# Performance work log

Hardware: AMD Instinct MI355X
Metric: run time of the kernel (lower is better)

Reference implementation:

```python
import jax, jax.numpy as jnp
import numpy as np


def setup_inputs() -> dict:
    key = jax.random.key(0)
    ks = jax.random.split(key, 6)
    B, U, E, D, P = 8, 1024, 1024, 256, 256
    return {
        "u_enc": jax.random.normal(ks[0], (B, U, D), dtype=jnp.float32),
        "e_enc": jax.random.normal(ks[1], (B, E, D), dtype=jnp.float32),
        "pair_enc": jax.random.normal(ks[2], (B, U, E), dtype=jnp.float32),
        "ue_mask": jax.random.uniform(ks[3], (B, U, E), dtype=jnp.float32),
        "w_kernel": jax.random.normal(ks[4], (D, P), dtype=jnp.float32) / np.sqrt(D).astype(np.float32),
        "w_bias": jnp.zeros((P,), dtype=jnp.float32),
        "bpp_w": jnp.ones((), dtype=jnp.float32),
        "bpp_b": jnp.zeros((), dtype=jnp.float32),
    }


def reference(u_enc, e_enc, pair_enc, ue_mask, w_kernel, w_bias, bpp_w, bpp_b):
    # OuterProductUpdate: shared Dense projection of u and e, then outer product.
    u_p = u_enc @ w_kernel + w_bias            # [B,U,P]
    e_p = e_enc @ w_kernel + w_bias            # [B,E,P]
    op = ue_mask * jnp.einsum('bup,bep->bue', u_p, e_p)  # [B,U,E]
    # Sigmoid gate over pair features.
    mask = ue_mask * jax.nn.sigmoid(bpp_w * pair_enc + bpp_b + op)  # [B,U,E]
    # Original: (mask[...,None] * concat(u_rep, e_rep)).sum(axis=(-2,-3)).
    # Algebraically identical without the UxEx2D intermediate:
    #   concat( sum_{u,e} mask * u_enc[u],  sum_{u,e} mask * e_enc[e] )
    u_part = jnp.einsum('bue,bud->bd', mask, u_enc)  # [B,D]
    e_part = jnp.einsum('bue,bed->bd', mask, e_enc)  # [B,D]
    return jnp.concatenate([u_part, e_part], axis=-1)  # [B,2D]
```

## Files before the change

### kernel.cpp

```cpp
#include <hip/hip_runtime.h>

#define BDIM 8
#define UDIM 1024
#define EDIM 1024
#define DDIM 256
#define PDIM 256

typedef __attribute__((ext_vector_type(8))) short bf16x8;
typedef __attribute__((ext_vector_type(4))) float f32x4;

__device__ __forceinline__ short f2bf(float x) {
    unsigned u = __float_as_uint(x);
    unsigned r = (u + 0x7FFFu + ((u >> 16) & 1u)) >> 16;
    return (short)r;
}

__global__ __launch_bounds__(256) void prep_kernel(
    const float* __restrict__ w, ushort* __restrict__ wT,
    float* __restrict__ sums ,
    float* __restrict__ out, int out_size)
{
    int n = blockIdx.x, k = threadIdx.x;
    wT[(size_t)n * PDIM + k] = (ushort)f2bf(w[(size_t)k * PDIM + n]);
    int g = n * 256 + k;
    if (g < BDIM * UDIM + BDIM * EDIM) sums[g] = 0.f;
    if (g < out_size) out[g] = 0.f;
}

__global__ __launch_bounds__(256) void proj_kernel(
    const float* __restrict__ u_enc, const float* __restrict__ e_enc,
    const ushort* __restrict__ wT, const float* __restrict__ bias,
    ushort* __restrict__ u_p, ushort* __restrict__ e_p)
{
    int row0 = blockIdx.x * 64;
    int col0 = blockIdx.y * 64;
    const float* A; ushort* C;
    if (row0 < BDIM * UDIM) { A = u_enc; C = u_p; }
    else                    { A = e_enc; C = e_p; row0 -= BDIM * UDIM; }

    int tid  = threadIdx.x;
    int wave = tid >> 6, lane = tid & 63;
    int m = lane & 15, quad = lane >> 4;

    const float* aptr = A + (size_t)(row0 + wave * 16 + m) * DDIM + quad * 8;

    f32x4 acc[4] = {};

    #pragma unroll
    for (int k0 = 0; k0 < DDIM; k0 += 32) {
        float4 a0 = *(const float4*)(aptr + k0);
        float4 a1 = *(const float4*)(aptr + k0 + 4);
        bf16x8 af;
        af[0] = f2bf(a0.x); af[1] = f2bf(a0.y); af[2] = f2bf(a0.z); af[3] = f2bf(a0.w);
        af[4] = f2bf(a1.x); af[5] = f2bf(a1.y); af[6] = f2bf(a1.z); af[7] = f2bf(a1.w);
        #pragma unroll
        for (int nt = 0; nt < 4; ++nt) {
            bf16x8 bfr = *(const bf16x8*)(wT + (size_t)(col0 + nt * 16 + m) * DDIM + k0 + quad * 8);
            acc[nt] = __builtin_amdgcn_mfma_f32_16x16x32_bf16(af, bfr, acc[nt], 0, 0, 0);
        }
    }

    #pragma unroll
    for (int nt = 0; nt < 4; ++nt) {
        int col = col0 + nt * 16 + m;
        float bv = bias[col];
        #pragma unroll
        for (int r = 0; r < 4; ++r) {
            int row = row0 + wave * 16 + quad * 4 + r;
            C[(size_t)row * PDIM + col] = (ushort)f2bf(acc[nt][r] + bv);
        }
    }
}

__global__ __launch_bounds__(256) void fused_kernel(
    const ushort* __restrict__ u_p, const ushort* __restrict__ e_p,
    const float* __restrict__ pair_enc, const float* __restrict__ ue_mask,
    const float* __restrict__ bpp_w_p, const float* __restrict__ bpp_b_p,
    float* __restrict__ row_sums, float* __restrict__ col_sums)
{
    __shared__ float colred[4][64];

    int b  = blockIdx.y;
    int iu = blockIdx.x >> 4, ie = blockIdx.x & 15;
    int u0 = iu * 64, e0 = ie * 64;

    int tid  = threadIdx.x;
    int wave = tid >> 6, lane = tid & 63;
    int m = lane & 15, quad = lane >> 4;

    const ushort* Au = u_p + (size_t)b * UDIM * PDIM + (size_t)(u0 + wave * 16 + m) * PDIM + quad * 8;
    const ushort* Be = e_p + (size_t)b * EDIM * PDIM + (size_t)(e0 + m) * PDIM + quad * 8;

    f32x4 acc[4] = {};

    #pragma unroll
    for (int k0 = 0; k0 < PDIM; k0 += 32) {
        bf16x8 af = *(const bf16x8*)(Au + k0);
        #pragma unroll
        for (int nt = 0; nt < 4; ++nt) {
            bf16x8 bfr = *(const bf16x8*)(Be + (size_t)nt * 16 * PDIM + k0);
            acc[nt] = __builtin_amdgcn_mfma_f32_16x16x32_bf16(af, bfr, acc[nt], 0, 0, 0);
        }
    }

    float bw = bpp_w_p[0], bb = bpp_b_p[0];
    const float* pm = pair_enc + (size_t)b * UDIM * EDIM;
    const float* mm = ue_mask  + (size_t)b * UDIM * EDIM;

    float rsum[4] = {0.f, 0.f, 0.f, 0.f};
    float csum[4] = {0.f, 0.f, 0.f, 0.f};
    #pragma unroll
    for (int r = 0; r < 4; ++r) {
        int row = u0 + wave * 16 + quad * 4 + r;
        #pragma unroll
        for (int nt = 0; nt < 4; ++nt) {
            int col = e0 + nt * 16 + m;
            size_t idx = (size_t)row * EDIM + col;
            float mv = mm[idx], pv = pm[idx];
            float arg = bw * pv + bb + mv * acc[nt][r];
            float s = mv / (1.f + __expf(-arg));
            rsum[r]  += s;
            csum[nt] += s;
        }
    }

    #pragma unroll
    for (int r = 0; r < 4; ++r) {
        float v = rsum[r];
        v += __shfl_xor(v, 1); v += __shfl_xor(v, 2);
        v += __shfl_xor(v, 4); v += __shfl_xor(v, 8);
        if (m == 0)
            atomicAdd(&row_sums[(size_t)b * UDIM + u0 + wave * 16 + quad * 4 + r], v);
    }

    #pragma unroll
    for (int nt = 0; nt < 4; ++nt) {
        float v = csum[nt];
        v += __shfl_xor(v, 16); v += __shfl_xor(v, 32);
        if (quad == 0) colred[wave][nt * 16 + m] = v;
    }
    __syncthreads();

    if (tid < 64) {
        float v = colred[0][tid] + colred[1][tid] + colred[2][tid] + colred[3][tid];
        atomicAdd(&col_sums[(size_t)b * EDIM + e0 + tid], v);
    }
}

__global__ __launch_bounds__(256) void finish_kernel(
    const float* __restrict__ u_enc, const float* __restrict__ e_enc,
    const float* __restrict__ row_sums, const float* __restrict__ col_sums,
    float* __restrict__ out)
{
    int b = blockIdx.x;
    int half = blockIdx.y;
    int chunk = blockIdx.z;
    int d = threadIdx.x;

    const float* enc = half ? e_enc : u_enc;
    const float* s   = half ? col_sums : row_sums;

    int base = chunk * 64;
    float acc = 0.f;
    #pragma unroll 4
    for (int u = 0; u < 64; ++u) {
        float sv = s[(size_t)b * UDIM + base + u];
        acc += sv * enc[(size_t)(b * UDIM + base + u) * DDIM + d];
    }
    atomicAdd(&out[(size_t)b * 2 * DDIM + half * DDIM + d], acc);
}

extern "C" void kernel_launch(void* const* d_in, const int* in_sizes, int n_in,
                              void* d_out, int out_size, void* d_ws, size_t ws_size,
                              hipStream_t stream)
{
    const float* u_enc    = (const float*)d_in[0];
    const float* e_enc    = (const float*)d_in[1];
    const float* pair_enc = (const float*)d_in[2];
    const float* ue_mask  = (const float*)d_in[3];
    const float* w_kernel = (const float*)d_in[4];
    const float* w_bias   = (const float*)d_in[5];
    const float* bpp_w    = (const float*)d_in[6];
    const float* bpp_b    = (const float*)d_in[7];
    float* out = (float*)d_out;

    ushort* u_p = (ushort*)d_ws;
    ushort* e_p = u_p + (size_t)BDIM * UDIM * PDIM;
    ushort* wT  = e_p + (size_t)BDIM * EDIM * PDIM;
    float* row_sums = (float*)(wT + (size_t)DDIM * PDIM);
    float* col_sums = row_sums + BDIM * UDIM;

    prep_kernel<<<dim3(256), 256, 0, stream>>>(w_kernel, wT, row_sums, out, out_size);

    proj_kernel<<<dim3(256, 4), 256, 0, stream>>>(u_enc, e_enc, wT, w_bias, u_p, e_p);

    fused_kernel<<<dim3(256, BDIM), 256, 0, stream>>>(u_p, e_p, pair_enc, ue_mask,
                                                      bpp_w, bpp_b, row_sums, col_sums);

    finish_kernel<<<dim3(BDIM, 2, 16), 256, 0, stream>>>(u_enc, e_enc, row_sums, col_sums, out);
}
```

Baseline: 180.0 us.

## Prefetch operands into registers and remap block order across all kernels

Every kernel now issues its global loads up front into register arrays. That covers the A rows in proj, the u_p fragments and the pair/mask tiles in fused, and the encoder rows in finish, so memory latency overlaps instead of serializing with the MFMA and sigmoid work. proj and fused use a 1D grid with swizzled block indices so the 8 XCDs each get a batch-local slice, which should improve L2 locality. prep transposes four columns per thread with float4 loads, and finish splits into more chunks for parallelism. The cost is higher register pressure and more atomics in finish.

```diff
diff --git a/kernel.cpp b/kernel.cpp
--- a/kernel.cpp
+++ b/kernel.cpp
@@ -20,10 +20,15 @@
     float* __restrict__ sums ,
     float* __restrict__ out, int out_size)
 {
-    int n = blockIdx.x, k = threadIdx.x;
-    wT[(size_t)n * PDIM + k] = (ushort)f2bf(w[(size_t)k * PDIM + n]);
-    int g = n * 256 + k;
-    if (g < BDIM * UDIM + BDIM * EDIM) sums[g] = 0.f;
+    int k  = threadIdx.x;
+    int n0 = blockIdx.x * 4;
+    float4 wv = *(const float4*)(w + (size_t)k * PDIM + n0);
+    wT[(size_t)(n0 + 0) * DDIM + k] = (ushort)f2bf(wv.x);
+    wT[(size_t)(n0 + 1) * DDIM + k] = (ushort)f2bf(wv.y);
+    wT[(size_t)(n0 + 2) * DDIM + k] = (ushort)f2bf(wv.z);
+    wT[(size_t)(n0 + 3) * DDIM + k] = (ushort)f2bf(wv.w);
+    int g = blockIdx.x * 256 + k;
+    sums[g] = 0.f;
     if (g < out_size) out[g] = 0.f;
 }
 
@@ -32,8 +37,11 @@
     const ushort* __restrict__ wT, const float* __restrict__ bias,
     ushort* __restrict__ u_p, ushort* __restrict__ e_p)
 {
-    int row0 = blockIdx.x * 64;
-    int col0 = blockIdx.y * 64;
+    int bid  = blockIdx.x;
+    int lin  = (bid & 7) * 128 + (bid >> 3);
+    int row0 = (lin >> 2) * 64;
+    int col0 = (lin & 3) * 64;
+
     const float* A; ushort* C;
     if (row0 < BDIM * UDIM) { A = u_enc; C = u_p; }
     else                    { A = e_enc; C = e_p; row0 -= BDIM * UDIM; }
@@ -44,15 +52,22 @@
 
     const float* aptr = A + (size_t)(row0 + wave * 16 + m) * DDIM + quad * 8;
 
+    float4 a[16];
+    #pragma unroll
+    for (int i = 0; i < 8; ++i) {
+        a[2 * i]     = *(const float4*)(aptr + 32 * i);
+        a[2 * i + 1] = *(const float4*)(aptr + 32 * i + 4);
+    }
+
     f32x4 acc[4] = {};
-
-    #pragma unroll
-    for (int k0 = 0; k0 < DDIM; k0 += 32) {
-        float4 a0 = *(const float4*)(aptr + k0);
-        float4 a1 = *(const float4*)(aptr + k0 + 4);
+    #pragma unroll
+    for (int i = 0; i < 8; ++i) {
         bf16x8 af;
-        af[0] = f2bf(a0.x); af[1] = f2bf(a0.y); af[2] = f2bf(a0.z); af[3] = f2bf(a0.w);
-        af[4] = f2bf(a1.x); af[5] = f2bf(a1.y); af[6] = f2bf(a1.z); af[7] = f2bf(a1.w);
+        af[0] = f2bf(a[2*i].x);   af[1] = f2bf(a[2*i].y);
+        af[2] = f2bf(a[2*i].z);   af[3] = f2bf(a[2*i].w);
+        af[4] = f2bf(a[2*i+1].x); af[5] = f2bf(a[2*i+1].y);
+        af[6] = f2bf(a[2*i+1].z); af[7] = f2bf(a[2*i+1].w);
+        int k0 = 32 * i;
         #pragma unroll
         for (int nt = 0; nt < 4; ++nt) {
             bf16x8 bfr = *(const bf16x8*)(wT + (size_t)(col0 + nt * 16 + m) * DDIM + k0 + quad * 8);
@@ -80,8 +95,10 @@
 {
     __shared__ float colred[4][64];
 
-    int b  = blockIdx.y;
-    int iu = blockIdx.x >> 4, ie = blockIdx.x & 15;
+    int bid  = blockIdx.x;
+    int b    = bid & 7;
+    int tile = bid >> 3;
+    int iu = tile >> 4, ie = tile & 15;
     int u0 = iu * 64, e0 = ie * 64;
 
     int tid  = threadIdx.x;
@@ -91,32 +108,45 @@
     const ushort* Au = u_p + (size_t)b * UDIM * PDIM + (size_t)(u0 + wave * 16 + m) * PDIM + quad * 8;
     const ushort* Be = e_p + (size_t)b * EDIM * PDIM + (size_t)(e0 + m) * PDIM + quad * 8;
 
+    bf16x8 af[8];
+    #pragma unroll
+    for (int i = 0; i < 8; ++i) af[i] = *(const bf16x8*)(Au + 32 * i);
+
+    float bw = bpp_w_p[0], bb = bpp_b_p[0];
+
     f32x4 acc[4] = {};
-
-    #pragma unroll
-    for (int k0 = 0; k0 < PDIM; k0 += 32) {
-        bf16x8 af = *(const bf16x8*)(Au + k0);
-        #pragma unroll
-        for (int nt = 0; nt < 4; ++nt) {
-            bf16x8 bfr = *(const bf16x8*)(Be + (size_t)nt * 16 * PDIM + k0);
-            acc[nt] = __builtin_amdgcn_mfma_f32_16x16x32_bf16(af, bfr, acc[nt], 0, 0, 0);
-        }
-    }
-
-    float bw = bpp_w_p[0], bb = bpp_b_p[0];
+    #pragma unroll
+    for (int i = 0; i < 8; ++i) {
+        #pragma unroll
+        for (int nt = 0; nt < 4; ++nt) {
+            bf16x8 bfr = *(const bf16x8*)(Be + (size_t)nt * 16 * PDIM + 32 * i);
+            acc[nt] = __builtin_amdgcn_mfma_f32_16x16x32_bf16(af[i], bfr, acc[nt], 0, 0, 0);
+        }
+    }
+
     const float* pm = pair_enc + (size_t)b * UDIM * EDIM;
     const float* mm = ue_mask  + (size_t)b * UDIM * EDIM;
 
+    __builtin_amdgcn_sched_barrier(0);
+    float mvv[16], pvv[16];
+    #pragma unroll
+    for (int r = 0; r < 4; ++r) {
+        size_t rowoff = (size_t)(u0 + wave * 16 + quad * 4 + r) * EDIM + e0 + m;
+        #pragma unroll
+        for (int nt = 0; nt < 4; ++nt) {
+            mvv[r * 4 + nt] = mm[rowoff + nt * 16];
+            pvv[r * 4 + nt] = pm[rowoff + nt * 16];
+        }
+    }
+    __builtin_amdgcn_sched_barrier(0);
+
     float rsum[4] = {0.f, 0.f, 0.f, 0.f};
     float csum[4] = {0.f, 0.f, 0.f, 0.f};
     #pragma unroll
     for (int r = 0; r < 4; ++r) {
-        int row = u0 + wave * 16 + quad * 4 + r;
-        #pragma unroll
-        for (int nt = 0; nt < 4; ++nt) {
-            int col = e0 + nt * 16 + m;
-            size_t idx = (size_t)row * EDIM + col;
-            float mv = mm[idx], pv = pm[idx];
+        #pragma unroll
+        for (int nt = 0; nt < 4; ++nt) {
+            float mv = mvv[r * 4 + nt], pv = pvv[r * 4 + nt];
             float arg = bw * pv + bb + mv * acc[nt][r];
             float s = mv / (1.f + __expf(-arg));
             rsum[r]  += s;
@@ -160,13 +190,17 @@
     const float* enc = half ? e_enc : u_enc;
     const float* s   = half ? col_sums : row_sums;
 
-    int base = chunk * 64;
+    int base = chunk * 16;
+    float ev[16];
+    #pragma unroll
+    for (int j = 0; j < 16; ++j)
+        ev[j] = enc[(size_t)(b * UDIM + base + j) * DDIM + d];
+
     float acc = 0.f;
-    #pragma unroll 4
-    for (int u = 0; u < 64; ++u) {
-        float sv = s[(size_t)b * UDIM + base + u];
-        acc += sv * enc[(size_t)(b * UDIM + base + u) * DDIM + d];
-    }
+    #pragma unroll
+    for (int j = 0; j < 16; ++j)
+        acc += s[(size_t)b * UDIM + base + j] * ev[j];
+
     atomicAdd(&out[(size_t)b * 2 * DDIM + half * DDIM + d], acc);
 }
 
@@ -190,12 +224,12 @@
     float* row_sums = (float*)(wT + (size_t)DDIM * PDIM);
     float* col_sums = row_sums + BDIM * UDIM;
 
-    prep_kernel<<<dim3(256), 256, 0, stream>>>(w_kernel, wT, row_sums, out, out_size);
-
-    proj_kernel<<<dim3(256, 4), 256, 0, stream>>>(u_enc, e_enc, wT, w_bias, u_p, e_p);
-
-    fused_kernel<<<dim3(256, BDIM), 256, 0, stream>>>(u_p, e_p, pair_enc, ue_mask,
-                                                      bpp_w, bpp_b, row_sums, col_sums);
-
-    finish_kernel<<<dim3(BDIM, 2, 16), 256, 0, stream>>>(u_enc, e_enc, row_sums, col_sums, out);
-}
+    prep_kernel<<<dim3(64), 256, 0, stream>>>(w_kernel, wT, row_sums, out, out_size);
+
+    proj_kernel<<<dim3(1024), 256, 0, stream>>>(u_enc, e_enc, wT, w_bias, u_p, e_p);
+
+    fused_kernel<<<dim3(2048), 256, 0, stream>>>(u_p, e_p, pair_enc, ue_mask,
+                                                 bpp_w, bpp_b, row_sums, col_sums);
+
+    finish_kernel<<<dim3(BDIM, 2, 64), 256, 0, stream>>>(u_enc, e_enc, row_sums, col_sums, out);
+}
```

Result: no change. 180.6 us (+0.3%).
